# Kernel optimization log

Hardware: AMD Instinct MI355X
Metric: run time of the kernel (lower is better)

Reference implementation:

```python
import jax, jax.numpy as jnp
import numpy as np

S = 32  # spatial_size
EPS = 1e-8

def _adaptive_avg_pool(x, s):
    b, c, h, w = x.shape
    kh, kw = h // s, w // s
    return x.reshape(b, c, s, kh, s, kw).mean(axis=(3, 5))

def _gram_cosine(x):
    # x: [B, C, s, s] -> rows: [B*s*s, C]
    b, c, s, _ = x.shape
    rows = x.reshape(b, c, s * s).transpose(0, 2, 1).reshape(b * s * s, c)
    norms = jnp.sqrt(jnp.sum(rows * rows, axis=-1, keepdims=True))
    xn = rows / jnp.maximum(norms, EPS)
    return xn @ xn.T  # [N, N]

def setup_inputs() -> dict:
    key = jax.random.key(0)
    k1, k2 = jax.random.split(key)
    p1 = jax.random.normal(k1, (8, 64, 128, 128), dtype=jnp.float32)
    p2 = jax.random.normal(k2, (8, 64, 128, 128), dtype=jnp.float32)
    return {"p1": p1, "p2": p2}

def reference(p1, p2):
    sim_a = _gram_cosine(_adaptive_avg_pool(p1, S))
    sim_b = _gram_cosine(_adaptive_avg_pool(p2, S))
    return jnp.mean((sim_a - sim_b) ** 2)
```

## Files before the change

### kernel.cpp

```cpp
#include <hip/hip_runtime.h>

typedef float f4 __attribute__((ext_vector_type(4)));
typedef float f2 __attribute__((ext_vector_type(2)));

#define PAD 68
#define NPART 256
#define PART_STRIDE 12288


__global__ __launch_bounds__(1024) void fused_gram_kernel(
    const float* __restrict__ p1, const float* __restrict__ p2,
    float* __restrict__ partials, unsigned* __restrict__ cnt)
{
    __shared__ float la[32 * PAD];
    __shared__ float lb[32 * PAD];
    __shared__ float nred[64][17];
    __shared__ float sa[32], sb[32];
    const int t  = threadIdx.x;
    const int b  = blockIdx.x >> 5;
    const int oi = blockIdx.x & 31;

    if (blockIdx.x == 0 && t == 0) *cnt = 0u;

    #pragma unroll
    for (int k = 0; k < 2; ++k) {
        const int idx = k * 1024 + t;
        const int c   = idx >> 5;
        const int oj  = idx & 31;
        const long off = (long)((b * 64 + c) * 128 + oi * 4) * 128 + oj * 4;
        const float* s1 = p1 + off;
        const float* s2 = p2 + off;
        f4 va = *(const f4*)(s1) + *(const f4*)(s1 + 128)
              + *(const f4*)(s1 + 256) + *(const f4*)(s1 + 384);
        f4 vb = *(const f4*)(s2) + *(const f4*)(s2 + 128)
              + *(const f4*)(s2 + 256) + *(const f4*)(s2 + 384);
        la[oj * PAD + c] = ((va[0] + va[1]) + (va[2] + va[3])) * 0.0625f;
        lb[oj * PAD + c] = ((vb[0] + vb[1]) + (vb[2] + vb[3])) * 0.0625f;
    }
    __syncthreads();

    {
        const int r = t & 31, g = t >> 5;
        const int m = g >> 4, q = g & 15;
        const float* src = m ? lb : la;
        float ss = 0.f;
        #pragma unroll
        for (int j = 0; j < 4; ++j) {
            const float v = src[r * PAD + q * 4 + j];
            ss = fmaf(v, v, ss);
        }
        nred[m * 32 + r][q] = ss;
    }
    __syncthreads();
    if (t < 64) {
        const int m = t >> 5, r = t & 31;
        float ss = 0.f;
        #pragma unroll
        for (int q = 0; q < 16; ++q) ss += nred[m * 32 + r][q];
        const float rs = 1.0f / fmaxf(sqrtf(ss), 1e-8f);
        if (m) sb[r] = rs; else sa[r] = rs;
    }
    __syncthreads();

    #pragma unroll
    for (int k = 0; k < 2; ++k) {
        const int idx = k * 1024 + t;
        const int c = idx >> 5, oj = idx & 31;
        la[oj * PAD + c] *= sa[oj];
        lb[oj * PAD + c] *= sb[oj];
    }
    __syncthreads();

    const int c1 = (t >> 5) * 2;
    const int c2 = (t & 31) * 2;
    f2 aa0 = {}, aa1 = {}, ab0 = {}, ab1 = {}, bb0 = {}, bb1 = {};

    #pragma unroll 8
    for (int r = 0; r < 32; ++r) {
        const f2 a1 = *(const f2*)&la[r * PAD + c1];
        const f2 a2 = *(const f2*)&la[r * PAD + c2];
        const f2 b1 = *(const f2*)&lb[r * PAD + c1];
        const f2 b2 = *(const f2*)&lb[r * PAD + c2];
        aa0 += a2 * a1[0];  aa1 += a2 * a1[1];
        ab0 += b2 * a1[0];  ab1 += b2 * a1[1];
        bb0 += b2 * b1[0];  bb1 += b2 * b1[1];
    }

    float* P = partials + (long)blockIdx.x * PART_STRIDE;
    *(f2*)&P[0 * 4096 + (c1    ) * 64 + c2] = aa0;
    *(f2*)&P[0 * 4096 + (c1 + 1) * 64 + c2] = aa1;
    *(f2*)&P[1 * 4096 + (c1    ) * 64 + c2] = ab0;
    *(f2*)&P[1 * 4096 + (c1 + 1) * 64 + c2] = ab1;
    *(f2*)&P[2 * 4096 + (c1    ) * 64 + c2] = bb0;
    *(f2*)&P[2 * 4096 + (c1 + 1) * 64 + c2] = bb1;
}

__global__ __launch_bounds__(256) void reduce_kernel(
    const float* __restrict__ partials, float* __restrict__ bpart,
    unsigned* __restrict__ cnt, float* __restrict__ out)
{
    __shared__ float red[3][16][17];
    __shared__ float vred[16];
    __shared__ float fr[256];
    __shared__ unsigned last_flag;
    const int t  = threadIdx.x;
    const int el = t & 15;
    const int pc = t >> 4;
    const int e  = blockIdx.x * 16 + el;

    float saa = 0.f, sab = 0.f, sbb = 0.f;
    #pragma unroll 4
    for (int i = 0; i < 16; ++i) {
        const float* P = partials + (long)(pc * 16 + i) * PART_STRIDE;
        saa += P[e];
        sab += P[4096 + e];
        sbb += P[8192 + e];
    }
    red[0][el][pc] = saa; red[1][el][pc] = sab; red[2][el][pc] = sbb;
    __syncthreads();

    if (t < 16) {
        float a = 0.f, m = 0.f, bv = 0.f;
        #pragma unroll
        for (int p = 0; p < 16; ++p) {
            a  += red[0][t][p];
            m  += red[1][t][p];
            bv += red[2][t][p];
        }
        vred[t] = fmaf(a, a, fmaf(bv, bv, -2.0f * (m * m)));
    }
    __syncthreads();

    if (t == 0) {
        float s = 0.f;
        #pragma unroll
        for (int i = 0; i < 16; ++i) s += vred[i];
        __hip_atomic_store(&bpart[blockIdx.x], s, __ATOMIC_RELEASE,
                           __HIP_MEMORY_SCOPE_AGENT);
        unsigned old = __hip_atomic_fetch_add(cnt, 1u, __ATOMIC_ACQ_REL,
                                              __HIP_MEMORY_SCOPE_AGENT);
        last_flag = (old == NPART - 1) ? 1u : 0u;
    }
    __syncthreads();

    if (last_flag) {
        fr[t] = __hip_atomic_load(&bpart[t], __ATOMIC_ACQUIRE,
                                  __HIP_MEMORY_SCOPE_AGENT);
        __syncthreads();
        for (int s2 = 128; s2 > 0; s2 >>= 1) {
            if (t < s2) fr[t] += fr[t + s2];
            __syncthreads();
        }
        if (t == 0) out[0] = fr[0] * (1.0f / 67108864.0f);
    }
}

extern "C" void kernel_launch(void* const* d_in, const int* in_sizes, int n_in,
                              void* d_out, int out_size, void* d_ws, size_t ws_size,
                              hipStream_t stream)
{
    const float* p1 = (const float*)d_in[0];
    const float* p2 = (const float*)d_in[1];
    float* ws       = (float*)d_ws;
    float* partials = ws;
    float* bpart    = ws + (long)NPART * PART_STRIDE;
    unsigned* cnt   = (unsigned*)(bpart + NPART);

    fused_gram_kernel<<<NPART, 1024, 0, stream>>>(p1, p2, partials, cnt);
    reduce_kernel   <<<NPART, 256, 0, stream>>>(partials, bpart, cnt, (float*)d_out);
}
```

Before: 35.19 us.

## Split pooling into separate wide kernel and use wave-shuffle row normalization

The fused gram kernel's pooling stage moves into its own kernel with 1024 blocks of 256 threads. Each block pools one (tensor, batch, channel) plane into a channel-major pooled buffer, which spreads the 64 MiB input read across more blocks and gives contiguous accesses. The gram kernel then loads the small pooled tile with vector loads and normalizes each row with a 64-lane xor-shuffle reduction, replacing the shared-memory partial-sum reduction and removing two barriers. The cost is an extra kernel launch and a round trip of the pooled data through global memory.

```diff
diff --git a/kernel.cpp b/kernel.cpp
--- a/kernel.cpp
+++ b/kernel.cpp
@@ -8,66 +8,71 @@
 #define PART_STRIDE 12288
 
 
-__global__ __launch_bounds__(1024) void fused_gram_kernel(
+__global__ __launch_bounds__(256) void pool_kernel(
     const float* __restrict__ p1, const float* __restrict__ p2,
-    float* __restrict__ partials, unsigned* __restrict__ cnt)
+    float* __restrict__ pooled, unsigned* __restrict__ cnt)
+{
+    const int t = threadIdx.x;
+    if (blockIdx.x == 0 && t == 0) *cnt = 0u;
+    const int blk = blockIdx.x;
+    const int m   = blk >> 9;
+    const int bc  = blk & 511;
+    const int b   = bc >> 6;
+    const int c   = bc & 63;
+    const float* src = (m ? p2 : p1) + (long)bc * 16384;
+    float* dst = pooled + (long)m * 524288 + (long)c * 8192 + b * 1024;
+
+    #pragma unroll
+    for (int k = 0; k < 4; ++k) {
+        const int o  = k * 256 + t;
+        const int oi = o >> 5, oj = o & 31;
+        const float* s = src + oi * 512 + oj * 4;
+        f4 v = *(const f4*)(s) + *(const f4*)(s + 128)
+             + *(const f4*)(s + 256) + *(const f4*)(s + 384);
+        dst[o] = ((v[0] + v[1]) + (v[2] + v[3])) * 0.0625f;
+    }
+}
+
+__global__ __launch_bounds__(1024) void gram_kernel(
+    const float* __restrict__ pooled, float* __restrict__ partials)
 {
     __shared__ float la[32 * PAD];
     __shared__ float lb[32 * PAD];
-    __shared__ float nred[64][17];
-    __shared__ float sa[32], sb[32];
     const int t  = threadIdx.x;
     const int b  = blockIdx.x >> 5;
     const int oi = blockIdx.x & 31;
 
-    if (blockIdx.x == 0 && t == 0) *cnt = 0u;
-
-    #pragma unroll
-    for (int k = 0; k < 2; ++k) {
-        const int idx = k * 1024 + t;
-        const int c   = idx >> 5;
-        const int oj  = idx & 31;
-        const long off = (long)((b * 64 + c) * 128 + oi * 4) * 128 + oj * 4;
-        const float* s1 = p1 + off;
-        const float* s2 = p2 + off;
-        f4 va = *(const f4*)(s1) + *(const f4*)(s1 + 128)
-              + *(const f4*)(s1 + 256) + *(const f4*)(s1 + 384);
-        f4 vb = *(const f4*)(s2) + *(const f4*)(s2 + 128)
-              + *(const f4*)(s2 + 256) + *(const f4*)(s2 + 384);
-        la[oj * PAD + c] = ((va[0] + va[1]) + (va[2] + va[3])) * 0.0625f;
-        lb[oj * PAD + c] = ((vb[0] + vb[1]) + (vb[2] + vb[3])) * 0.0625f;
+    {
+        const int oj4 = t & 7;
+        const int c   = (t >> 3) & 63;
+        const int m   = t >> 9;
+        const f4 v = *(const f4*)&pooled[(long)m * 524288 + (long)c * 8192
+                                         + b * 1024 + oi * 32 + oj4 * 4];
+        float* dst = (m ? lb : la) + c;
+        dst[(oj4 * 4 + 0) * PAD] = v[0];
+        dst[(oj4 * 4 + 1) * PAD] = v[1];
+        dst[(oj4 * 4 + 2) * PAD] = v[2];
+        dst[(oj4 * 4 + 3) * PAD] = v[3];
     }
     __syncthreads();
 
     {
-        const int r = t & 31, g = t >> 5;
-        const int m = g >> 4, q = g & 15;
-        const float* src = m ? lb : la;
-        float ss = 0.f;
+        const int w = t >> 6, l = t & 63;
         #pragma unroll
         for (int j = 0; j < 4; ++j) {
-            const float v = src[r * PAD + q * 4 + j];
-            ss = fmaf(v, v, ss);
+            const int rs = j * 16 + w;
+            const int m = rs >> 5, r = rs & 31;
+            float* rowp = (m ? lb : la) + r * PAD;
+            const float v = rowp[l];
+            float ss = v * v;
+            ss += __shfl_xor(ss, 1);
+            ss += __shfl_xor(ss, 2);
+            ss += __shfl_xor(ss, 4);
+            ss += __shfl_xor(ss, 8);
+            ss += __shfl_xor(ss, 16);
+            ss += __shfl_xor(ss, 32);
+            rowp[l] = v * (1.0f / fmaxf(sqrtf(ss), 1e-8f));
         }
-        nred[m * 32 + r][q] = ss;
-    }
-    __syncthreads();
-    if (t < 64) {
-        const int m = t >> 5, r = t & 31;
-        float ss = 0.f;
-        #pragma unroll
-        for (int q = 0; q < 16; ++q) ss += nred[m * 32 + r][q];
-        const float rs = 1.0f / fmaxf(sqrtf(ss), 1e-8f);
-        if (m) sb[r] = rs; else sa[r] = rs;
-    }
-    __syncthreads();
-
-    #pragma unroll
-    for (int k = 0; k < 2; ++k) {
-        const int idx = k * 1024 + t;
-        const int c = idx >> 5, oj = idx & 31;
-        la[oj * PAD + c] *= sa[oj];
-        lb[oj * PAD + c] *= sb[oj];
     }
     __syncthreads();
 
@@ -120,14 +125,14 @@
     __syncthreads();
 
     if (t < 16) {
-        float a = 0.f, m = 0.f, bv = 0.f;
+        float a = 0.f, mm = 0.f, bv = 0.f;
         #pragma unroll
         for (int p = 0; p < 16; ++p) {
             a  += red[0][t][p];
-            m  += red[1][t][p];
+            mm += red[1][t][p];
             bv += red[2][t][p];
         }
-        vred[t] = fmaf(a, a, fmaf(bv, bv, -2.0f * (m * m)));
+        vred[t] = fmaf(a, a, fmaf(bv, bv, -2.0f * (mm * mm)));
     }
     __syncthreads();
 
@@ -162,10 +167,12 @@
     const float* p1 = (const float*)d_in[0];
     const float* p2 = (const float*)d_in[1];
     float* ws       = (float*)d_ws;
-    float* partials = ws;
-    float* bpart    = ws + (long)NPART * PART_STRIDE;
-    unsigned* cnt   = (unsigned*)(bpart + NPART);
+    float* pooled   = ws;
+    float* partials = ws + 1048576;
+    float* bpart    = ws + 4194304;
+    unsigned* cnt   = (unsigned*)(ws + 4194816);
 
-    fused_gram_kernel<<<NPART, 1024, 0, stream>>>(p1, p2, partials, cnt);
-    reduce_kernel   <<<NPART, 256, 0, stream>>>(partials, bpart, cnt, (float*)d_out);
+    pool_kernel  <<<1024, 256, 0, stream>>>(p1, p2, pooled, cnt);
+    gram_kernel  <<<NPART, 1024, 0, stream>>>(pooled, partials);
+    reduce_kernel<<<NPART, 256, 0, stream>>>(partials, bpart, cnt, (float*)d_out);
 }
```

After: 37.69 us. 7.1% more time.
